# Performance work log

Measured on AMD Instinct MI355X. Metric: run time of the kernel, lower is better.

## Reference

```python
import jax, jax.numpy as jnp
import numpy as np

N_NODES = 50000
NUM_FEA = 213
HID, IN_HEAD = 16, 12
OUT_DIM, OUT_HEAD = 8, 8
NEG_SLOPE = 0.2


def gat_conv(x, W, att_src, att_dst, bias, src, dst, H, C):
    # x: [N, F] -> h: [N, H, C]
    N = x.shape[0]
    h = (x @ W).reshape(N, H, C)
    a_s = jnp.sum(h * att_src, axis=-1)  # [N, H]
    a_d = jnp.sum(h * att_dst, axis=-1)  # [N, H]
    e = jax.nn.leaky_relu(a_s[src] + a_d[dst], NEG_SLOPE)  # [E, H]
    # segment softmax over incoming edges of each dst node
    m = jax.ops.segment_max(e, dst, num_segments=N)
    ex = jnp.exp(e - m[dst])
    denom = jax.ops.segment_sum(ex, dst, num_segments=N)
    alpha = ex / denom[dst]  # [E, H]
    out = jax.ops.segment_sum(h[src] * alpha[:, :, None], dst, num_segments=N)
    return out.reshape(N, H * C) + bias


def setup_inputs() -> dict:
    key = jax.random.key(0)
    ks = jax.random.split(key, 16)
    E = 800000
    P = 16384
    features = jax.random.normal(ks[0], (N_NODES, NUM_FEA), dtype=jnp.float32)
    edge_index = jax.random.randint(ks[1], (2, E), 0, N_NODES, dtype=jnp.int32)
    node1_index = jax.random.randint(ks[2], (P,), 0, N_NODES, dtype=jnp.int32)
    node2_index = jax.random.randint(ks[3], (P,), 0, N_NODES, dtype=jnp.int32)
    s1 = 1.0 / np.sqrt(NUM_FEA)
    s2 = 1.0 / np.sqrt(HID * IN_HEAD)
    s3 = 1.0 / np.sqrt(OUT_DIM * OUT_HEAD * 2)
    params = {
        'W1': jax.random.normal(ks[4], (NUM_FEA, IN_HEAD * HID), jnp.float32) * s1,
        'att_src1': jax.random.normal(ks[5], (IN_HEAD, HID), jnp.float32) * s1,
        'att_dst1': jax.random.normal(ks[6], (IN_HEAD, HID), jnp.float32) * s1,
        'b1': jnp.zeros((IN_HEAD * HID,), jnp.float32),
        'W2': jax.random.normal(ks[7], (IN_HEAD * HID, OUT_HEAD * OUT_DIM), jnp.float32) * s2,
        'att_src2': jax.random.normal(ks[8], (OUT_HEAD, OUT_DIM), jnp.float32) * s2,
        'att_dst2': jax.random.normal(ks[9], (OUT_HEAD, OUT_DIM), jnp.float32) * s2,
        'b2': jnp.zeros((OUT_HEAD * OUT_DIM,), jnp.float32),
        'linW': jax.random.normal(ks[10], (OUT_DIM * OUT_HEAD * 2, 2), jnp.float32) * s3,
        'linb': jnp.zeros((2,), jnp.float32),
    }
    return dict(features=features, edge_index=edge_index,
                node1_index=node1_index, node2_index=node2_index, **params)


def reference(features, edge_index, node1_index, node2_index,
              W1, att_src1, att_dst1, b1, W2, att_src2, att_dst2, b2, linW, linb):
    # eval mode: dropout(p=0.8) is identity
    N = features.shape[0]
    self_loops = jnp.arange(N, dtype=edge_index.dtype)
    src = jnp.concatenate([edge_index[0], self_loops])
    dst = jnp.concatenate([edge_index[1], self_loops])
    x = gat_conv(features, W1, att_src1, att_dst1, b1, src, dst, IN_HEAD, HID)
    x = jax.nn.elu(x)
    x = gat_conv(x, W2, att_src2, att_dst2, b2, src, dst, OUT_HEAD, OUT_DIM)
    x = jax.nn.elu(x)
    pair = jnp.concatenate([x[node1_index], x[node2_index]], axis=1)
    y_pred = jax.nn.sigmoid(pair @ linW + linb)
    return (y_pred, x)
```

## Files before the change

### kernel.cpp

```cpp
#include <hip/hip_runtime.h>
#include <hip/hip_bf16.h>

#define HID1 16
#define NHEAD1 12
#define F1 (HID1*NHEAD1)
#define HID2 8
#define NHEAD2 8
#define F2 (HID2*NHEAD2)
#define NUM_FEA 213
#define NEG_SLOPE 0.2f
#define KP 224
#define KP2 192
#define LDK 40
#define MROWS 128
#define NC1 224
#define NW2R 80
#define SLOTS 56
#define BINS 256
#define NPB 196
#define CAP 4096
#define FILLB 256
#define EPT 13

typedef __attribute__((ext_vector_type(8))) __bf16 bf16x8;
typedef __attribute__((ext_vector_type(4))) float floatx4;
typedef float floatx4u __attribute__((ext_vector_type(4), aligned(4)));
typedef unsigned short ushort_t;

static __device__ __forceinline__ unsigned short f2bf(float f) {
    unsigned u = __float_as_uint(f);
    unsigned r = (u + 0x7fffu + ((u >> 16) & 1u)) >> 16;
    return (unsigned short)r;
}
static __device__ __forceinline__ float lrelu(float e) {
    return e > 0.f ? e : NEG_SLOPE * e;
}
static __device__ __forceinline__ float elu(float v) {
    return v > 0.f ? v : (__expf(v) - 1.f);
}


__global__ __launch_bounds__(256) void prep_kernel(
        const float* __restrict__ W1, const float* __restrict__ as1w,
        const float* __restrict__ ad1w, ushort_t* __restrict__ Wt1,
        const float* __restrict__ W2, const float* __restrict__ as2w,
        const float* __restrict__ ad2w, ushort_t* __restrict__ Wt2,
        const int* __restrict__ ei, int* __restrict__ binctr,
        unsigned* __restrict__ binbuf, int E, int Etot, int nwb) {
    int b = (int)blockIdx.x;
    int tid = threadIdx.x;
    if (b >= nwb) {
        __shared__ int hist[BINS];
        __shared__ int cur[BINS];
        int fb = b - nwb;
        if (tid < BINS) hist[tid] = 0;
        __syncthreads();
        unsigned stash[EPT];
        int base_e = fb * 256 + tid;
#pragma unroll
        for (int i = 0; i < EPT; i++) {
            int e = base_e + i * (FILLB * 256);
            unsigned pk = 0xffffffffu;
            if (e < Etot) {
                int s, d;
                if (e < E) { s = ei[e]; d = ei[E + e]; } else { s = e - E; d = s; }
                pk = (unsigned)s | ((unsigned)d << 16);
                atomicAdd(&hist[(unsigned)d / NPB], 1);
            }
            stash[i] = pk;
        }
        __syncthreads();
        if (tid < BINS) cur[tid] = atomicAdd(&binctr[tid], hist[tid]);
        __syncthreads();
#pragma unroll
        for (int i = 0; i < EPT; i++) {
            unsigned pk = stash[i];
            if (pk != 0xffffffffu) {
                int d = (int)(pk >> 16);
                int bin = (int)((unsigned)d / NPB);
                int dl = d - bin * NPB;
                int r = atomicAdd(&cur[bin], 1);
                if (r < CAP)
                    binbuf[(long)bin * CAP + r] = (pk & 0xffffu) | ((unsigned)dl << 16);
            }
        }
        return;
    }
    int j = b * 256 + tid;
    if (j < NC1 * KP) {
        int n = j / KP, k = j - n * KP;
        float v = 0.f;
        if (k < NUM_FEA) {
            if (n < 192) {
                v = W1[(long)k * F1 + n];
            } else if (n < 204) {
                int hd = n - 192;
                for (int c = 0; c < HID1; c++)
                    v += W1[(long)k * F1 + hd * HID1 + c] * as1w[hd * HID1 + c];
            } else if (n < 216) {
                int hd = n - 204;
                for (int c = 0; c < HID1; c++)
                    v += W1[(long)k * F1 + hd * HID1 + c] * ad1w[hd * HID1 + c];
            }
        }
        Wt1[j] = f2bf(v);
    } else {
        int j2 = j - NC1 * KP;
        if (j2 < NW2R * KP2) {
            int n = j2 / KP2, k = j2 - n * KP2;
            float v;
            if (n < 64) {
                v = W2[(long)k * F2 + n];
            } else if (n < 72) {
                int hd = n - 64;
                v = 0.f;
                for (int c = 0; c < HID2; c++)
                    v += W2[(long)k * F2 + hd * HID2 + c] * as2w[hd * HID2 + c];
            } else {
                int hd = n - 72;
                v = 0.f;
                for (int c = 0; c < HID2; c++)
                    v += W2[(long)k * F2 + hd * HID2 + c] * ad2w[hd * HID2 + c];
            }
            Wt2[j2] = f2bf(v);
        }
    }
}


__global__ __launch_bounds__(256) void binsort_kernel(
        const unsigned* __restrict__ binbuf, const int* __restrict__ binctr,
        ushort_t* __restrict__ esrcp, int* __restrict__ cnt, int N) {
    __shared__ int lcnt[NPB];
    int b = blockIdx.x, tid = threadIdx.x;
    if (tid < NPB) lcnt[tid] = 0;
    __syncthreads();
    int cntb = binctr[b];
    if (cntb > CAP) cntb = CAP;
    const unsigned* seg = binbuf + (long)b * CAP;
    for (int t = tid; t < cntb; t += 256) {
        unsigned u = seg[t];
        int s = (int)(u & 0xffffu);
        int dl = (int)(u >> 16);
        int slot = atomicAdd(&lcnt[dl], 1);
        if (slot < SLOTS)
            esrcp[(long)(b * NPB + dl) * SLOTS + slot] = (ushort_t)s;
    }
    __syncthreads();
    int d = b * NPB + tid;
    if (tid < NPB && d < N) cnt[d] = lcnt[tid];
}


static __device__ __forceinline__ void stageA(ushort_t* dst, const float* xp,
                                              bool ok, int col) {
    union { int4 q; ushort_t u[8]; } pk;
    if (ok && col + 8 <= NUM_FEA) {
        floatx4u a = *(const floatx4u*)(xp + col);
        floatx4u c = *(const floatx4u*)(xp + col + 4);
#pragma unroll
        for (int j = 0; j < 4; j++) { pk.u[j] = f2bf(a[j]); pk.u[4 + j] = f2bf(c[j]); }
    } else {
#pragma unroll
        for (int j = 0; j < 8; j++) {
            float v = (ok && col + j < NUM_FEA) ? xp[col + j] : 0.f;
            pk.u[j] = f2bf(v);
        }
    }
    *(int4*)dst = pk.q;
}

__global__ __launch_bounds__(256) void gemm1_kernel(
        const float* __restrict__ X, const ushort_t* __restrict__ Wt,
        ushort_t* __restrict__ Hout, float* __restrict__ as_, float* __restrict__ ad_,
        int N) {
    __shared__ ushort_t As[MROWS * LDK];
    __shared__ ushort_t Bs[NC1 * LDK];
    int tid = threadIdx.x;
    int wave = tid >> 6, lane = tid & 63;
    int q = lane >> 4, l16 = lane & 15;
    int wm = (wave >> 1) * 64;
    int wn = (wave & 1) * 112;
    long row0 = (long)blockIdx.x * MROWS;

    int r0 = tid >> 2, ksl = (tid & 3) * 8;
    long gr0 = row0 + r0, gr1 = gr0 + 64;
    bool ok0 = gr0 < N, ok1 = gr1 < N;
    const float* xp0 = X + gr0 * NUM_FEA;
    const float* xp1 = X + gr1 * NUM_FEA;
    ushort_t* lds0 = &As[r0 * LDK + ksl];
    ushort_t* lds1 = &As[(r0 + 64) * LDK + ksl];

    floatx4 acc[4][7] = {};

    for (int k0 = 0; k0 < KP; k0 += 32) {
        stageA(lds0, xp0, ok0, k0 + ksl);
        stageA(lds1, xp1, ok1, k0 + ksl);
#pragma unroll
        for (int p = 0; p < 4; p++) {
            int idx = p * 256 + tid;
            if (idx < NC1 * 4) {
                int r = idx >> 2, ks = (idx & 3) * 8;
                *(int4*)&Bs[r * LDK + ks] = *(const int4*)&Wt[(long)r * KP + k0 + ks];
            }
        }
        __syncthreads();
        bf16x8 af[4], bfr[7];
#pragma unroll
        for (int rt = 0; rt < 4; rt++)
            af[rt] = *(const bf16x8*)&As[(wm + rt * 16 + l16) * LDK + q * 8];
#pragma unroll
        for (int ct = 0; ct < 7; ct++)
            bfr[ct] = *(const bf16x8*)&Bs[(wn + ct * 16 + l16) * LDK + q * 8];
#pragma unroll
        for (int rt = 0; rt < 4; rt++)
#pragma unroll
            for (int ct = 0; ct < 7; ct++)
                acc[rt][ct] = __builtin_amdgcn_mfma_f32_16x16x32_bf16(af[rt], bfr[ct], acc[rt][ct], 0, 0, 0);
        __syncthreads();
    }
#pragma unroll
    for (int rt = 0; rt < 4; rt++) {
#pragma unroll
        for (int r = 0; r < 4; r++) {
            long grow = row0 + wm + rt * 16 + q * 4 + r;
            if (grow < N) {
#pragma unroll
                for (int ct = 0; ct < 7; ct++) {
                    int col = wn + ct * 16 + l16;
                    float v = acc[rt][ct][r];
                    if (col < 192)      Hout[grow * F1 + col] = f2bf(v);
                    else if (col < 204) as_[grow * NHEAD1 + col - 192] = v;
                    else if (col < 216) ad_[grow * NHEAD1 + col - 204] = v;
                }
            }
        }
    }
}


__global__ __launch_bounds__(256) void gemm2_mfma(const ushort_t* __restrict__ Xbf,
                                                  const ushort_t* __restrict__ Wt,
                                                  ushort_t* __restrict__ Hout,
                                                  float* __restrict__ as_,
                                                  float* __restrict__ ad_, int N) {
    __shared__ ushort_t As[MROWS * LDK];
    __shared__ ushort_t Bs[96 * LDK];
    int tid = threadIdx.x;
    int wave = tid >> 6, lane = tid & 63;
    int q = lane >> 4, l16 = lane & 15;
    int wm = (wave >> 1) * 64;
    int wn = (wave & 1) * 48;
    long row0 = (long)blockIdx.x * MROWS;

    floatx4 acc[4][3] = {};

    for (int k0 = 0; k0 < KP2; k0 += 32) {
#pragma unroll
        for (int p = 0; p < 2; p++) {
            int idx = p * 256 + tid;
            int r = idx >> 2, ks = (idx & 3) * 8;
            *(int4*)&As[r * LDK + ks] = *(const int4*)&Xbf[(row0 + r) * KP2 + k0 + ks];
        }
#pragma unroll
        for (int p = 0; p < 2; p++) {
            int idx = p * 256 + tid;
            if (idx < 96 * 4) {
                int r = idx >> 2, ks = (idx & 3) * 8;
                int4 z = {0, 0, 0, 0};
                *(int4*)&Bs[r * LDK + ks] = (r < NW2R) ? *(const int4*)&Wt[(long)r * KP2 + k0 + ks] : z;
            }
        }
        __syncthreads();
        bf16x8 af[4], bfr[3];
#pragma unroll
        for (int rt = 0; rt < 4; rt++)
            af[rt] = *(const bf16x8*)&As[(wm + rt * 16 + l16) * LDK + q * 8];
#pragma unroll
        for (int ct = 0; ct < 3; ct++)
            bfr[ct] = *(const bf16x8*)&Bs[(wn + ct * 16 + l16) * LDK + q * 8];
#pragma unroll
        for (int rt = 0; rt < 4; rt++)
#pragma unroll
            for (int ct = 0; ct < 3; ct++)
                acc[rt][ct] = __builtin_amdgcn_mfma_f32_16x16x32_bf16(af[rt], bfr[ct], acc[rt][ct], 0, 0, 0);
        __syncthreads();
    }
#pragma unroll
    for (int rt = 0; rt < 4; rt++) {
#pragma unroll
        for (int r = 0; r < 4; r++) {
            long grow = row0 + wm + rt * 16 + q * 4 + r;
            if (grow < N) {
#pragma unroll
                for (int ct = 0; ct < 3; ct++) {
                    int col = wn + ct * 16 + l16;
                    float v = acc[rt][ct][r];
                    if (col < 64)      Hout[grow * F2 + col] = f2bf(v);
                    else if (col < 72) as_[grow * NHEAD2 + col - 64] = v;
                    else if (col < 80) ad_[grow * NHEAD2 + col - 72] = v;
                }
            }
        }
    }
}


__global__ __launch_bounds__(256) void gather1_kernel(const int* __restrict__ cnt,
                                                      const ushort_t* __restrict__ esrcp,
                                                      const float* __restrict__ as_,
                                                      const float* __restrict__ ad_,
                                                      const ushort_t* __restrict__ h,
                                                      const float* __restrict__ bias,
                                                      ushort_t* __restrict__ xout, int N) {
    int d = blockIdx.x * 4 + (threadIdx.x >> 6);
    if (d >= N) return;
    int l = threadIdx.x & 63;
    int jc = l < 48 ? l : 47;
    int hj = jc >> 2;
    int e0 = l / 12, h0 = l - e0 * 12;
    int l64 = l + 64;
    int e1 = l64 / 12, h1 = l64 - e1 * 12;
    int deg = cnt[d]; if (deg > SLOTS) deg = SLOTS;
    int beg = d * SLOTS, end = beg + deg;
    float adv0 = ad_[d * NHEAD1 + h0];
    float adv1 = ad_[d * NHEAD1 + h1];
    float4 b4 = ((const float4*)bias)[jc];
    const ushort_t* hcol = h + 4 * jc;

    float acc0 = 0.f, acc1 = 0.f, acc2 = 0.f, acc3 = 0.f, accd = 0.f;

    for (int p = beg; p < end; p += 8) {
        int pp = p + (l & 7);
        int s_l = (int)esrcp[pp < end ? pp : beg];
        int s_e[8];
#pragma unroll
        for (int i = 0; i < 8; i++) s_e[i] = __shfl(s_l, i, 64);
        uint2 g[8];
#pragma unroll
        for (int i = 0; i < 8; i++)
            g[i] = *(const uint2*)(hcol + (long)s_e[i] * F1);
        int sq0 = __shfl(s_l, e0, 64);
        int sq1 = __shfl(s_l, e1, 64);
        float a0v = as_[sq0 * NHEAD1 + h0];
        float a1v = as_[sq1 * NHEAD1 + h1];
        float w0 = (p + e0 < end) ? __expf(lrelu(a0v + adv0)) : 0.f;
        float w1 = (e1 < 8 && p + e1 < end) ? __expf(lrelu(a1v + adv1)) : 0.f;
#pragma unroll
        for (int i = 0; i < 8; i++) {
            float wi;
            if (i <= 4) {
                wi = __shfl(w0, i * 12 + hj, 64);
            } else if (i == 5) {
                float wa = __shfl(w0, 60 + hj, 64);
                int srcb = hj >= 4 ? hj - 4 : 0;
                float wb = __shfl(w1, srcb, 64);
                wi = (hj < 4) ? wa : wb;
            } else {
                wi = __shfl(w1, i * 12 + hj - 64, 64);
            }
            unsigned x = g[i].x, y = g[i].y;
            acc0 += wi * __uint_as_float(x << 16);
            acc1 += wi * __uint_as_float(x & 0xffff0000u);
            acc2 += wi * __uint_as_float(y << 16);
            acc3 += wi * __uint_as_float(y & 0xffff0000u);
            accd += wi;
        }
    }
    if (l < 48) {
        float v0 = elu(acc0 / accd + b4.x);
        float v1 = elu(acc1 / accd + b4.y);
        float v2 = elu(acc2 / accd + b4.z);
        float v3 = elu(acc3 / accd + b4.w);
        uint2 outp;
        outp.x = (unsigned)f2bf(v0) | ((unsigned)f2bf(v1) << 16);
        outp.y = (unsigned)f2bf(v2) | ((unsigned)f2bf(v3) << 16);
        *(uint2*)(xout + (long)d * F1 + 4 * l) = outp;
    }
}


__global__ __launch_bounds__(256) void gather2_kernel(const int* __restrict__ cnt,
                                                      const ushort_t* __restrict__ esrcp,
                                                      const float* __restrict__ as_,
                                                      const float* __restrict__ ad_,
                                                      const ushort_t* __restrict__ h,
                                                      const float* __restrict__ bias,
                                                      float* __restrict__ xout, int N) {
    int d = blockIdx.x * 4 + (threadIdx.x >> 6);
    if (d >= N) return;
    int l = threadIdx.x & 63;
    int cg = l & 15;
    int hj = cg >> 1;
    int e_lo = l >> 4;
    int ie0 = l >> 3, hq = l & 7;
    int ie1 = 8 + ie0;
    int deg = cnt[d]; if (deg > SLOTS) deg = SLOTS;
    int beg = d * SLOTS, end = beg + deg;
    float advq = ad_[d * NHEAD2 + hq];
    const ushort_t* hcol = h + 4 * cg;

    float acc0 = 0.f, acc1 = 0.f, acc2 = 0.f, acc3 = 0.f, accd = 0.f;

    for (int p = beg; p < end; p += 16) {
        int pp = p + (l & 15);
        int s_l = (int)esrcp[pp < end ? pp : beg];
        int se[4];
#pragma unroll
        for (int k = 0; k < 4; k++) se[k] = __shfl(s_l, e_lo + 4 * k, 64);
        uint2 g[4];
#pragma unroll
        for (int k = 0; k < 4; k++)
            g[k] = *(const uint2*)(hcol + (long)se[k] * F2);
        int sq0 = __shfl(s_l, ie0, 64);
        int sq1 = __shfl(s_l, ie1, 64);
        float a0v = as_[sq0 * NHEAD2 + hq];
        float a1v = as_[sq1 * NHEAD2 + hq];
        float w0d = (p + ie0 < end) ? __expf(lrelu(a0v + advq)) : 0.f;
        float w1d = (p + ie1 < end) ? __expf(lrelu(a1v + advq)) : 0.f;
#pragma unroll
        for (int k = 0; k < 4; k++) {
            int i = e_lo + 4 * k;
            float wk = (k < 2) ? __shfl(w0d, i * 8 + hj, 64)
                               : __shfl(w1d, i * 8 + hj - 64, 64);
            unsigned x = g[k].x, y = g[k].y;
            acc0 += wk * __uint_as_float(x << 16);
            acc1 += wk * __uint_as_float(x & 0xffff0000u);
            acc2 += wk * __uint_as_float(y << 16);
            acc3 += wk * __uint_as_float(y & 0xffff0000u);
            accd += wk;
        }
    }
    acc0 += __shfl_xor(acc0, 16, 64); acc0 += __shfl_xor(acc0, 32, 64);
    acc1 += __shfl_xor(acc1, 16, 64); acc1 += __shfl_xor(acc1, 32, 64);
    acc2 += __shfl_xor(acc2, 16, 64); acc2 += __shfl_xor(acc2, 32, 64);
    acc3 += __shfl_xor(acc3, 16, 64); acc3 += __shfl_xor(acc3, 32, 64);
    accd += __shfl_xor(accd, 16, 64); accd += __shfl_xor(accd, 32, 64);
    if (l < 16) {
        float4 b4 = ((const float4*)bias)[cg];
        float4 outp;
        outp.x = elu(acc0 / accd + b4.x);
        outp.y = elu(acc1 / accd + b4.y);
        outp.z = elu(acc2 / accd + b4.z);
        outp.w = elu(acc3 / accd + b4.w);
        *(float4*)(xout + (long)d * F2 + 4 * cg) = outp;
    }
}


__global__ void pair_kernel(const float* __restrict__ x, const int* __restrict__ n1,
                            const int* __restrict__ n2, const float* __restrict__ linW,
                            const float* __restrict__ linb, float* __restrict__ y, int P) {
    int idx = blockIdx.x * blockDim.x + threadIdx.x;
    if (idx >= P) return;
    const float4* xa = (const float4*)(x + (long)n1[idx] * F2);
    const float4* xb = (const float4*)(x + (long)n2[idx] * F2);
    float a0 = linb[0], a1 = linb[1];
#pragma unroll
    for (int k4 = 0; k4 < F2 / 4; k4++) {
        float4 v = xa[k4];
        int k = k4 * 4;
        a0 += v.x * linW[2 * k] + v.y * linW[2 * (k + 1)] + v.z * linW[2 * (k + 2)] + v.w * linW[2 * (k + 3)];
        a1 += v.x * linW[2 * k + 1] + v.y * linW[2 * (k + 1) + 1] + v.z * linW[2 * (k + 2) + 1] + v.w * linW[2 * (k + 3) + 1];
    }
#pragma unroll
    for (int k4 = 0; k4 < F2 / 4; k4++) {
        float4 v = xb[k4];
        int k = F2 + k4 * 4;
        a0 += v.x * linW[2 * k] + v.y * linW[2 * (k + 1)] + v.z * linW[2 * (k + 2)] + v.w * linW[2 * (k + 3)];
        a1 += v.x * linW[2 * k + 1] + v.y * linW[2 * (k + 1) + 1] + v.z * linW[2 * (k + 2) + 1] + v.w * linW[2 * (k + 3) + 1];
    }
    y[2 * idx]     = 1.f / (1.f + __expf(-a0));
    y[2 * idx + 1] = 1.f / (1.f + __expf(-a1));
}


extern "C" void kernel_launch(void* const* d_in, const int* in_sizes, int n_in,
                              void* d_out, int out_size, void* d_ws, size_t ws_size,
                              hipStream_t stream) {
    const float* features = (const float*)d_in[0];
    const int*   ei       = (const int*)d_in[1];
    const int*   n1       = (const int*)d_in[2];
    const int*   n2       = (const int*)d_in[3];
    const float* W1       = (const float*)d_in[4];
    const float* att_s1   = (const float*)d_in[5];
    const float* att_d1   = (const float*)d_in[6];
    const float* b1       = (const float*)d_in[7];
    const float* W2       = (const float*)d_in[8];
    const float* att_s2   = (const float*)d_in[9];
    const float* att_d2   = (const float*)d_in[10];
    const float* b2       = (const float*)d_in[11];
    const float* linW     = (const float*)d_in[12];
    const float* linb     = (const float*)d_in[13];

    const int N = in_sizes[0] / NUM_FEA;
    const int E = in_sizes[1] / 2;
    const int P = in_sizes[2];
    const int Etot = E + N;

    const int nblk = (N + MROWS - 1) / MROWS;
    const int nwb = (NC1 * KP + NW2R * KP2 + 255) / 256;

    float* ws = (float*)d_ws;
    long o = 0;
    float* h1r  = ws + o; o += (long)N * F1 / 2;
    float* x1r  = ws + o; o += (long)N * F1 / 2;
    float* as1  = ws + o; o += (long)N * NHEAD1;
    float* ad1  = ws + o; o += (long)N * NHEAD1;
    float* h2r  = ws + o; o += (long)N * F2 / 2;
    float* as2  = ws + o; o += (long)N * NHEAD2;
    float* ad2  = ws + o; o += (long)N * NHEAD2;
    float* w1r  = ws + o; o += ((long)NC1 * KP + 1) / 2;
    float* w2r  = ws + o; o += ((long)NW2R * KP2 + 1) / 2;
    float* esr  = ws + o; o += ((long)N * SLOTS + 1) / 2;
    unsigned* binbuf = (unsigned*)(ws + o); o += (long)BINS * CAP;
    int* binctr = (int*)(ws + o); o += BINS;
    int* cnt  = (int*)(ws + o); o += N;

    ushort_t* h1b   = (ushort_t*)h1r;
    ushort_t* x1bf  = (ushort_t*)x1r;
    ushort_t* h2b   = (ushort_t*)h2r;
    ushort_t* Wt1   = (ushort_t*)w1r;
    ushort_t* Wt2   = (ushort_t*)w2r;
    ushort_t* esrcp = (ushort_t*)esr;

    float* y_out = (float*)d_out;
    float* x_out = (float*)d_out + (long)2 * P;

    hipMemsetAsync(binctr, 0, (size_t)BINS * sizeof(int), stream);

    prep_kernel<<<nwb + FILLB, 256, 0, stream>>>(
        W1, att_s1, att_d1, Wt1, W2, att_s2, att_d2, Wt2,
        ei, binctr, binbuf, E, Etot, nwb);

    binsort_kernel<<<BINS, 256, 0, stream>>>(binbuf, binctr, esrcp, cnt, N);

    gemm1_kernel<<<nblk, 256, 0, stream>>>(features, Wt1, h1b, as1, ad1, N);

    gather1_kernel<<<(N + 3) / 4, 256, 0, stream>>>(cnt, esrcp, as1, ad1, h1b, b1, x1bf, N);

    gemm2_mfma<<<nblk, 256, 0, stream>>>(x1bf, Wt2, h2b, as2, ad2, N);
    gather2_kernel<<<(N + 3) / 4, 256, 0, stream>>>(cnt, esrcp, as2, ad2, h2b, b2, x_out, N);

    pair_kernel<<<(P + 255) / 256, 256, 0, stream>>>(x_out, n1, n2, linW, linb, y_out, P);
}
```

Before: 271.6 us.

## Fuse binsort into gemm1 launch and use packed FMA with 32-bit offsets in gathers

The bin-sort work now runs as extra blocks appended to the gemm1 grid, so it overlaps with the GEMM and one kernel launch is removed. The two gather kernels compute gather addresses with 32-bit unsigned byte offsets instead of 64-bit multiplies. They also accumulate into float2 vectors so the compiler can emit packed FMA instructions. The risks are a larger grid that mixes two block types, which could change occupancy, and a 32-bit offset that must stay in range. It stays in range for N=50000.

```diff
diff --git a/kernel.cpp b/kernel.cpp
--- a/kernel.cpp
+++ b/kernel.cpp
@@ -24,6 +24,7 @@
 
 typedef __attribute__((ext_vector_type(8))) __bf16 bf16x8;
 typedef __attribute__((ext_vector_type(4))) float floatx4;
+typedef __attribute__((ext_vector_type(2))) float floatx2;
 typedef float floatx4u __attribute__((ext_vector_type(4), aligned(4)));
 typedef unsigned short ushort_t;
 
@@ -128,30 +129,6 @@
 }
 
 
-__global__ __launch_bounds__(256) void binsort_kernel(
-        const unsigned* __restrict__ binbuf, const int* __restrict__ binctr,
-        ushort_t* __restrict__ esrcp, int* __restrict__ cnt, int N) {
-    __shared__ int lcnt[NPB];
-    int b = blockIdx.x, tid = threadIdx.x;
-    if (tid < NPB) lcnt[tid] = 0;
-    __syncthreads();
-    int cntb = binctr[b];
-    if (cntb > CAP) cntb = CAP;
-    const unsigned* seg = binbuf + (long)b * CAP;
-    for (int t = tid; t < cntb; t += 256) {
-        unsigned u = seg[t];
-        int s = (int)(u & 0xffffu);
-        int dl = (int)(u >> 16);
-        int slot = atomicAdd(&lcnt[dl], 1);
-        if (slot < SLOTS)
-            esrcp[(long)(b * NPB + dl) * SLOTS + slot] = (ushort_t)s;
-    }
-    __syncthreads();
-    int d = b * NPB + tid;
-    if (tid < NPB && d < N) cnt[d] = lcnt[tid];
-}
-
-
 static __device__ __forceinline__ void stageA(ushort_t* dst, const float* xp,
                                               bool ok, int col) {
     union { int4 q; ushort_t u[8]; } pk;
@@ -170,13 +147,36 @@
     *(int4*)dst = pk.q;
 }
 
-__global__ __launch_bounds__(256) void gemm1_kernel(
+__global__ __launch_bounds__(256) void gemm1_bs_kernel(
         const float* __restrict__ X, const ushort_t* __restrict__ Wt,
         ushort_t* __restrict__ Hout, float* __restrict__ as_, float* __restrict__ ad_,
-        int N) {
+        const unsigned* __restrict__ binbuf, const int* __restrict__ binctr,
+        ushort_t* __restrict__ esrcp, int* __restrict__ cnt,
+        int N, int nblk_gemm) {
     __shared__ ushort_t As[MROWS * LDK];
     __shared__ ushort_t Bs[NC1 * LDK];
+    __shared__ int lcnt[NPB];
     int tid = threadIdx.x;
+    if ((int)blockIdx.x >= nblk_gemm) {
+        int b = (int)blockIdx.x - nblk_gemm;
+        if (tid < NPB) lcnt[tid] = 0;
+        __syncthreads();
+        int cntb = binctr[b];
+        if (cntb > CAP) cntb = CAP;
+        const unsigned* seg = binbuf + (long)b * CAP;
+        for (int t = tid; t < cntb; t += 256) {
+            unsigned u = seg[t];
+            int s = (int)(u & 0xffffu);
+            int dl = (int)(u >> 16);
+            int slot = atomicAdd(&lcnt[dl], 1);
+            if (slot < SLOTS)
+                esrcp[(long)(b * NPB + dl) * SLOTS + slot] = (ushort_t)s;
+        }
+        __syncthreads();
+        int d = b * NPB + tid;
+        if (tid < NPB && d < N) cnt[d] = lcnt[tid];
+        return;
+    }
     int wave = tid >> 6, lane = tid & 63;
     int q = lane >> 4, l16 = lane & 15;
     int wm = (wave >> 1) * 64;
@@ -326,9 +326,10 @@
     float adv0 = ad_[d * NHEAD1 + h0];
     float adv1 = ad_[d * NHEAD1 + h1];
     float4 b4 = ((const float4*)bias)[jc];
-    const ushort_t* hcol = h + 4 * jc;
-
-    float acc0 = 0.f, acc1 = 0.f, acc2 = 0.f, acc3 = 0.f, accd = 0.f;
+    const char* hcol = (const char*)(h + 4 * jc);
+
+    floatx2 a01 = {0.f, 0.f}, a23 = {0.f, 0.f};
+    float accd = 0.f;
 
     for (int p = beg; p < end; p += 8) {
         int pp = p + (l & 7);
@@ -338,8 +339,10 @@
         for (int i = 0; i < 8; i++) s_e[i] = __shfl(s_l, i, 64);
         uint2 g[8];
 #pragma unroll
-        for (int i = 0; i < 8; i++)
-            g[i] = *(const uint2*)(hcol + (long)s_e[i] * F1);
+        for (int i = 0; i < 8; i++) {
+            unsigned off = (unsigned)s_e[i] * (unsigned)(F1 * 2);
+            g[i] = *(const uint2*)(hcol + off);
+        }
         int sq0 = __shfl(s_l, e0, 64);
         int sq1 = __shfl(s_l, e1, 64);
         float a0v = as_[sq0 * NHEAD1 + h0];
@@ -360,18 +363,22 @@
                 wi = __shfl(w1, i * 12 + hj - 64, 64);
             }
             unsigned x = g[i].x, y = g[i].y;
-            acc0 += wi * __uint_as_float(x << 16);
-            acc1 += wi * __uint_as_float(x & 0xffff0000u);
-            acc2 += wi * __uint_as_float(y << 16);
-            acc3 += wi * __uint_as_float(y & 0xffff0000u);
+            floatx2 h01, h23, w2;
+            h01.x = __uint_as_float(x << 16);
+            h01.y = __uint_as_float(x & 0xffff0000u);
+            h23.x = __uint_as_float(y << 16);
+            h23.y = __uint_as_float(y & 0xffff0000u);
+            w2.x = wi; w2.y = wi;
+            a01 += w2 * h01;
+            a23 += w2 * h23;
             accd += wi;
         }
     }
     if (l < 48) {
-        float v0 = elu(acc0 / accd + b4.x);
-        float v1 = elu(acc1 / accd + b4.y);
-        float v2 = elu(acc2 / accd + b4.z);
-        float v3 = elu(acc3 / accd + b4.w);
+        float v0 = elu(a01.x / accd + b4.x);
+        float v1 = elu(a01.y / accd + b4.y);
+        float v2 = elu(a23.x / accd + b4.z);
+        float v3 = elu(a23.y / accd + b4.w);
         uint2 outp;
         outp.x = (unsigned)f2bf(v0) | ((unsigned)f2bf(v1) << 16);
         outp.y = (unsigned)f2bf(v2) | ((unsigned)f2bf(v3) << 16);
@@ -398,9 +405,10 @@
     int deg = cnt[d]; if (deg > SLOTS) deg = SLOTS;
     int beg = d * SLOTS, end = beg + deg;
     float advq = ad_[d * NHEAD2 + hq];
-    const ushort_t* hcol = h + 4 * cg;
-
-    float acc0 = 0.f, acc1 = 0.f, acc2 = 0.f, acc3 = 0.f, accd = 0.f;
+    const char* hcol = (const char*)(h + 4 * cg);
+
+    floatx2 a01 = {0.f, 0.f}, a23 = {0.f, 0.f};
+    float accd = 0.f;
 
     for (int p = beg; p < end; p += 16) {
         int pp = p + (l & 15);
@@ -410,8 +418,10 @@
         for (int k = 0; k < 4; k++) se[k] = __shfl(s_l, e_lo + 4 * k, 64);
         uint2 g[4];
 #pragma unroll
-        for (int k = 0; k < 4; k++)
-            g[k] = *(const uint2*)(hcol + (long)se[k] * F2);
+        for (int k = 0; k < 4; k++) {
+            unsigned off = (unsigned)se[k] * (unsigned)(F2 * 2);
+            g[k] = *(const uint2*)(hcol + off);
+        }
         int sq0 = __shfl(s_l, ie0, 64);
         int sq1 = __shfl(s_l, ie1, 64);
         float a0v = as_[sq0 * NHEAD2 + hq];
@@ -424,25 +434,29 @@
             float wk = (k < 2) ? __shfl(w0d, i * 8 + hj, 64)
                                : __shfl(w1d, i * 8 + hj - 64, 64);
             unsigned x = g[k].x, y = g[k].y;
-            acc0 += wk * __uint_as_float(x << 16);
-            acc1 += wk * __uint_as_float(x & 0xffff0000u);
-            acc2 += wk * __uint_as_float(y << 16);
-            acc3 += wk * __uint_as_float(y & 0xffff0000u);
+            floatx2 h01, h23, w2;
+            h01.x = __uint_as_float(x << 16);
+            h01.y = __uint_as_float(x & 0xffff0000u);
+            h23.x = __uint_as_float(y << 16);
+            h23.y = __uint_as_float(y & 0xffff0000u);
+            w2.x = wk; w2.y = wk;
+            a01 += w2 * h01;
+            a23 += w2 * h23;
             accd += wk;
         }
     }
-    acc0 += __shfl_xor(acc0, 16, 64); acc0 += __shfl_xor(acc0, 32, 64);
-    acc1 += __shfl_xor(acc1, 16, 64); acc1 += __shfl_xor(acc1, 32, 64);
-    acc2 += __shfl_xor(acc2, 16, 64); acc2 += __shfl_xor(acc2, 32, 64);
-    acc3 += __shfl_xor(acc3, 16, 64); acc3 += __shfl_xor(acc3, 32, 64);
-    accd += __shfl_xor(accd, 16, 64); accd += __shfl_xor(accd, 32, 64);
+    a01.x += __shfl_xor(a01.x, 16, 64); a01.x += __shfl_xor(a01.x, 32, 64);
+    a01.y += __shfl_xor(a01.y, 16, 64); a01.y += __shfl_xor(a01.y, 32, 64);
+    a23.x += __shfl_xor(a23.x, 16, 64); a23.x += __shfl_xor(a23.x, 32, 64);
+    a23.y += __shfl_xor(a23.y, 16, 64); a23.y += __shfl_xor(a23.y, 32, 64);
+    accd  += __shfl_xor(accd, 16, 64);  accd  += __shfl_xor(accd, 32, 64);
     if (l < 16) {
         float4 b4 = ((const float4*)bias)[cg];
         float4 outp;
-        outp.x = elu(acc0 / accd + b4.x);
-        outp.y = elu(acc1 / accd + b4.y);
-        outp.z = elu(acc2 / accd + b4.z);
-        outp.w = elu(acc3 / accd + b4.w);
+        outp.x = elu(a01.x / accd + b4.x);
+        outp.y = elu(a01.y / accd + b4.y);
+        outp.z = elu(a23.x / accd + b4.z);
+        outp.w = elu(a23.y / accd + b4.w);
         *(float4*)(xout + (long)d * F2 + 4 * cg) = outp;
     }
 }
@@ -533,9 +547,8 @@
         W1, att_s1, att_d1, Wt1, W2, att_s2, att_d2, Wt2,
         ei, binctr, binbuf, E, Etot, nwb);
 
-    binsort_kernel<<<BINS, 256, 0, stream>>>(binbuf, binctr, esrcp, cnt, N);
-
-    gemm1_kernel<<<nblk, 256, 0, stream>>>(features, Wt1, h1b, as1, ad1, N);
+    gemm1_bs_kernel<<<nblk + BINS, 256, 0, stream>>>(
+        features, Wt1, h1b, as1, ad1, binbuf, binctr, esrcp, cnt, N, nblk);
 
     gather1_kernel<<<(N + 3) / 4, 256, 0, stream>>>(cnt, esrcp, as1, ad1, h1b, b1, x1bf, N);
 
```

Result: faster. 263.3 us (-3.1%).
